# Kernel tuning notes

Hardware: AMD Instinct MI355X
Metric: run time of the kernel (lower is better)

## Reference

```python
import jax, jax.numpy as jnp
import numpy as np

NODE_SIZE = 30000
REL_SIZE = 1000
TRIPLE_SIZE = 200000
DIM = 128
DEPTH = 2
BATCH = 2048
GAMMA = 3.0
LAMB, TAU = 30.0, 10.0


def glorot(k, shape):
    lim = np.sqrt(6.0 / (shape[-2] + shape[-1]))
    return jax.random.uniform(k, shape, minval=-lim, maxval=lim, dtype=jnp.float32)


def setup_inputs() -> dict:
    key = jax.random.key(0)
    ks = jax.random.split(key, 12)
    train_paris = jax.random.randint(ks[0], (BATCH, 2), 0, NODE_SIZE, dtype=jnp.int32)
    ent_adj = jax.random.randint(ks[1], (2, TRIPLE_SIZE), 0, NODE_SIZE, dtype=jnp.int32)
    rel_adj = jnp.stack([
        jax.random.randint(ks[2], (TRIPLE_SIZE,), 0, NODE_SIZE, dtype=jnp.int32),
        jax.random.randint(ks[3], (TRIPLE_SIZE,), 0, REL_SIZE, dtype=jnp.int32),
    ])
    adj_list = jax.random.randint(ks[4], (2, TRIPLE_SIZE), 0, NODE_SIZE, dtype=jnp.int32)
    r_index = jnp.stack([
        jnp.arange(TRIPLE_SIZE, dtype=jnp.int32),
        jax.random.randint(ks[5], (TRIPLE_SIZE,), 0, REL_SIZE, dtype=jnp.int32),
    ])
    r_val = jax.random.uniform(ks[6], (TRIPLE_SIZE,), dtype=jnp.float32)
    mask = jnp.ones((TRIPLE_SIZE,), jnp.float32)
    ent_emb = glorot(ks[7], (NODE_SIZE, DIM))
    rel_emb = glorot(ks[8], (REL_SIZE, DIM))
    attn_e = glorot(ks[9], (DEPTH, DIM, 1))
    attn_r = glorot(ks[10], (DEPTH, DIM, 1))
    return dict(train_paris=train_paris, ent_adj=ent_adj, rel_adj=rel_adj,
                adj_list=adj_list, r_index=r_index, r_val=r_val, mask=mask,
                ent_emb=ent_emb, rel_emb=rel_emb, attn_e=attn_e, attn_r=attn_r,
                node_size=NODE_SIZE, rel_size=REL_SIZE, triple_size=TRIPLE_SIZE)


def sparse_mean(adj, emb, num_rows):
    # torch.sparse.softmax over all-ones values == 1/deg per row, then sparse mm == mean aggregation
    rows, cols = adj[0], adj[1]
    s = jax.ops.segment_sum(emb[cols], rows, num_segments=num_rows)
    cnt = jax.ops.segment_sum(jnp.ones(rows.shape, emb.dtype), rows, num_segments=num_rows)
    return s / jnp.maximum(cnt, 1.0)[:, None]


def segment_softmax(logits, seg, num_segments):
    m = jax.lax.stop_gradient(jax.ops.segment_max(logits, seg, num_segments=num_segments))
    e = jnp.exp(logits - m[seg])
    z = jax.ops.segment_sum(e, seg, num_segments=num_segments)
    return e / z[seg]


def nr_gat(features, rel_emb, adj_list, r_index, r_val, attn_kernels, node_size, triple_size):
    # RREA-style NR_GraphAttention: relation-aware reflection + segment softmax attention
    feats = jnp.tanh(features)
    outs = [feats]
    # tri_rel[t] = sum_r r_val * rel_emb[r] for entries (t, r); here one relation per triple
    tri_rel = jax.ops.segment_sum(r_val[:, None] * rel_emb[r_index[1]], r_index[0],
                                  num_segments=triple_size)
    tri_rel = tri_rel / jnp.maximum(jnp.linalg.norm(tri_rel, axis=1, keepdims=True), 1e-12)
    rows, cols = adj_list[0], adj_list[1]
    for l in range(DEPTH):
        neighs = feats[cols]  # [T, D]
        # Householder reflection across normalized relation vector
        neighs = neighs - 2.0 * jnp.sum(neighs * tri_rel, axis=1, keepdims=True) * tri_rel
        att = jnp.squeeze(tri_rel @ attn_kernels[l], axis=-1)  # [T]
        w = segment_softmax(att, rows, node_size)
        feats = jnp.tanh(jax.ops.segment_sum(w[:, None] * neighs, rows, num_segments=node_size))
        outs.append(feats)
    return jnp.concatenate(outs, axis=1)  # [N, (depth+1)*D]


def align_loss(pairs, emb, node_size):
    l, r = pairs[:, 0], pairs[:, 1]
    l_emb, r_emb = emb[l], emb[r]
    pos = jnp.sum(jnp.square(l_emb - r_emb), axis=-1, keepdims=True)  # [B,1]
    emb_sq = jnp.sum(emb * emb, axis=1)  # [N]

    def sqdist(A):
        return jnp.sum(A * A, axis=1, keepdims=True) + emb_sq[None, :] - 2.0 * (A @ emb.T)

    b = pairs.shape[0]
    rows = jnp.arange(b)
    factor = jnp.ones((b, node_size), emb.dtype).at[rows, l].add(-1.0).at[rows, r].add(-1.0)

    def branch(neg):
        loss = (pos - neg + GAMMA) * factor
        mu = jax.lax.stop_gradient(jnp.mean(loss, axis=-1, keepdims=True))
        sd = jax.lax.stop_gradient(jnp.std(loss, axis=-1, keepdims=True))
        return jax.nn.logsumexp(LAMB * (loss - mu) / sd + TAU, axis=-1)

    return jnp.mean(branch(sqdist(l_emb)) + branch(sqdist(r_emb)))


def reference(train_paris, ent_adj, rel_adj, adj_list, r_index, r_val, mask,
              ent_emb, rel_emb, attn_e, attn_r, node_size, rel_size, triple_size):
    # gcn_forward: mean aggregation of entity / relation embeddings (sparse softmax of ones + spmm)
    ent_feature = sparse_mean(ent_adj, ent_emb, node_size)
    rel_feature = sparse_mean(rel_adj, rel_emb, node_size)
    e_out = nr_gat(ent_feature, rel_emb, adj_list, r_index, r_val, attn_e, node_size, triple_size)
    r_out = nr_gat(rel_feature, rel_emb, adj_list, r_index, r_val, attn_r, node_size, triple_size)
    out_feature = jnp.concatenate([e_out, r_out], axis=-1)  # [N, 2*(depth+1)*D]; dropout rate 0 -> identity
    return align_loss(train_paris, out_feature, node_size)
```

## Files before the change

kernel.cpp:

```cpp
#include <hip/hip_runtime.h>
#include <hip/hip_bf16.h>
#include <math.h>

#define N_NODE 30000
#define N_TRI  200000
#define DIM    128
#define OUTD   768
#define BATCH  2048
#define NROWA  4096
#define EPAD   30080
#define PADN   80
#define NTILE_E 235
#define NTILE_A 32
#define NCHB   16
#define NBLK_SCAN 118
#define TILE_ELEMS (128*OUTD)
#define KBLK_ELEMS (128*32)
#define GAMMA_C 3.0f
#define LAMB_C  30.0f
#define TAU_C   10.0f

typedef __attribute__((ext_vector_type(8)))  __bf16 bf16x8;
typedef __attribute__((ext_vector_type(4)))  __bf16 bf16x4;
typedef __attribute__((ext_vector_type(2)))  __bf16 bf16x2;
typedef __attribute__((ext_vector_type(8)))  _Float16 half8;
typedef __attribute__((ext_vector_type(4)))  float f32x4;

__device__ __forceinline__ float waveSum(float v){
#pragma unroll
  for (int m=1;m<64;m<<=1) v += __shfl_xor(v, m, 64);
  return v;
}
__device__ __forceinline__ float halfSum(float v){
#pragma unroll
  for (int m=1;m<32;m<<=1) v += __shfl_xor(v, m, 64);
  return v;
}

__device__ __forceinline__ void atomicMinF(float* a, float v){
  if (v >= 0.f) atomicMin((int*)a, __float_as_int(v));
  else          atomicMax((unsigned int*)a, __float_as_uint(v));
}

__device__ __forceinline__ void gl2lds16(const void* g, void* l){
  __builtin_amdgcn_global_load_lds(
      (const __attribute__((address_space(1))) char*)g,
      (__attribute__((address_space(3))) char*)l, 16, 0, 0);
}

__device__ __forceinline__ int swz_off(int r, int q){
  return r*32 + ((q ^ ((r>>1)&3))<<3);
}

__global__ void k_fill(float* __restrict__ p, long n, float v){
  long i = (long)blockIdx.x*blockDim.x + threadIdx.x;
  long st = (long)gridDim.x*blockDim.x;
  for (; i<n; i+=st) p[i]=v;
}

__global__ __launch_bounds__(256) void k_hist(const int* __restrict__ rows, int* __restrict__ cnt){
  int t = blockIdx.x*256 + threadIdx.x;
  if (t < N_TRI) atomicAdd(&cnt[rows[t]], 1);
}

__global__ __launch_bounds__(256) void k_scanA(
    const int* __restrict__ c0, const int* __restrict__ c1, const int* __restrict__ c2,
    int* __restrict__ r0, int* __restrict__ r1, int* __restrict__ r2,
    int* __restrict__ btot, int n){
  const int* cnt = blockIdx.y==0 ? c0 : (blockIdx.y==1 ? c1 : c2);
  int* rp        = blockIdx.y==0 ? r0 : (blockIdx.y==1 ? r1 : r2);
  __shared__ int buf[256];
  int i = blockIdx.x*256 + threadIdx.x;
  int v = (i<n) ? cnt[i] : 0;
  buf[threadIdx.x] = v;
  __syncthreads();
  for (int off=1; off<256; off<<=1){
    int t = (threadIdx.x>=off) ? buf[threadIdx.x-off] : 0;
    __syncthreads();
    buf[threadIdx.x] += t;
    __syncthreads();
  }
  if (i<n) rp[i] = buf[threadIdx.x] - v;
  if (threadIdx.x==255) btot[blockIdx.y*NBLK_SCAN + blockIdx.x] = buf[255];
}

__global__ __launch_bounds__(128) void k_scanB(int* __restrict__ btot,
    int* __restrict__ r0, int* __restrict__ r1, int* __restrict__ r2, int n){
  __shared__ int buf[128];
  int c = blockIdx.x;
  int v = (threadIdx.x < NBLK_SCAN) ? btot[c*NBLK_SCAN + threadIdx.x] : 0;
  buf[threadIdx.x] = v;
  __syncthreads();
  for (int off=1; off<128; off<<=1){
    int t = (threadIdx.x>=off) ? buf[threadIdx.x-off] : 0;
    __syncthreads();
    buf[threadIdx.x] += t;
    __syncthreads();
  }
  if (threadIdx.x < NBLK_SCAN) btot[c*NBLK_SCAN + threadIdx.x] = buf[threadIdx.x] - v;
  if (threadIdx.x == 127){
    int* rp = c==0 ? r0 : (c==1 ? r1 : r2);
    rp[n] = buf[127];
  }
}

__global__ __launch_bounds__(256) void k_scanC(
    int* __restrict__ r0, int* __restrict__ r1, int* __restrict__ r2,
    const int* __restrict__ btot, int n){
  int* rp = blockIdx.y==0 ? r0 : (blockIdx.y==1 ? r1 : r2);
  int i = blockIdx.x*256 + threadIdx.x;
  if (i<n) rp[i] += btot[blockIdx.y*NBLK_SCAN + blockIdx.x];
}

__global__ __launch_bounds__(256) void k_place(const int* __restrict__ rows, const int* __restrict__ vals,
                        const int* __restrict__ rowptr, int* __restrict__ cur, int* __restrict__ idx, int mode){
  int t = blockIdx.x*256 + threadIdx.x;
  if (t < N_TRI){
    int r = rows[t];
    int p = atomicAdd(&cur[r], 1);
    idx[rowptr[r] + p] = mode ? vals[t] : t;
  }
}

__global__ __launch_bounds__(256) void k_feat0(
    const int* __restrict__ rpE, const int* __restrict__ idxE,
    const int* __restrict__ rpR, const int* __restrict__ idxR,
    const float* __restrict__ ent_emb, const float* __restrict__ rel_emb,
    __bf16* __restrict__ outb){
  int wave = threadIdx.x>>6, lane = threadIdx.x&63;
  int i = blockIdx.x*4 + wave;
  if (i >= N_NODE) return;
  int bE = rpE[i], eE = rpE[i+1];
  int bR = rpR[i], eR = rpR[i+1];
  float2 aE = {0.f,0.f}, aR = {0.f,0.f};
  for (int k=bE; k<eE; ++k){
    int c = idxE[k];
    float2 v = *(const float2*)(ent_emb + (size_t)c*DIM + lane*2);
    aE.x += v.x; aE.y += v.y;
  }
  for (int k=bR; k<eR; ++k){
    int c = idxR[k];
    float2 v = *(const float2*)(rel_emb + (size_t)c*DIM + lane*2);
    aR.x += v.x; aR.y += v.y;
  }
  float ie = 1.f/fmaxf((float)(eE-bE), 1.f);
  float ir = 1.f/fmaxf((float)(eR-bR), 1.f);
  bf16x2 oE, oR;
  oE[0] = (__bf16)tanhf(aE.x*ie); oE[1] = (__bf16)tanhf(aE.y*ie);
  oR[0] = (__bf16)tanhf(aR.x*ir); oR[1] = (__bf16)tanhf(aR.y*ir);
  *(bf16x2*)(outb + (size_t)i*OUTD +   0 + lane*2) = oE;
  *(bf16x2*)(outb + (size_t)i*OUTD + 128 + lane*2) = oR;
}

__global__ __launch_bounds__(256) void k_trinorm(
    const int* __restrict__ ridx1, const float* __restrict__ rval,
    const float* __restrict__ rel_emb,
    __bf16* __restrict__ tri, const float* __restrict__ attnE,
    const float* __restrict__ attnR, float* __restrict__ att4){
  __shared__ float ak[4][DIM];
  int tid = threadIdx.x;
  for (int idx=tid; idx<4*DIM; idx+=256){
    int k = idx>>7, d = idx&127;
    ak[k][d] = (k<2) ? attnE[k*DIM + d] : attnR[(k-2)*DIM + d];
  }
  __syncthreads();
  int half = tid>>5, l31 = tid&31;
  int t = blockIdx.x*8 + half;
  if (t >= N_TRI) return;
  int rr = ridx1[t];
  float rv = rval[t];
  float4 v = *(const float4*)(rel_emb + (size_t)rr*DIM + l31*4);
  v.x *= rv; v.y *= rv; v.z *= rv; v.w *= rv;
  float ss = halfSum(v.x*v.x + v.y*v.y + v.z*v.z + v.w*v.w);
  float inv = 1.f/fmaxf(sqrtf(ss), 1e-12f);
  v.x *= inv; v.y *= inv; v.z *= inv; v.w *= inv;
  bf16x4 b; b[0]=(__bf16)v.x; b[1]=(__bf16)v.y; b[2]=(__bf16)v.z; b[3]=(__bf16)v.w;
  *(bf16x4*)(tri + (size_t)t*DIM + l31*4) = b;
#pragma unroll
  for (int k=0;k<4;k++){
    const float* a = &ak[k][l31*4];
    float p = halfSum(v.x*a[0] + v.y*a[1] + v.z*a[2] + v.w*a[3]);
    if (l31==0) att4[(size_t)k*N_TRI + t] = p;
  }
}

__global__ __launch_bounds__(256) void k_gat(
    const int* __restrict__ rowptr, const int* __restrict__ idx, const int* __restrict__ cols,
    const __bf16* __restrict__ tri,
    const float* __restrict__ attE, const float* __restrict__ attR,
    __bf16* __restrict__ outb, int inOff, int outOff){
  int wave = threadIdx.x>>6, lane = threadIdx.x&63;
  int i = blockIdx.x*4 + wave;
  if (i >= N_NODE) return;
  int l31 = lane&31;
  const float* att = (lane < 32) ? attE : attR;
  int beg = rowptr[i], end = rowptr[i+1];
  float a0=0.f, a1=0.f, a2=0.f, a3=0.f;
  if (end > beg){
    float z = 0.f;
    int t0 = idx[beg];
    int c0 = cols[t0];
    bf16x4 u4 = *(const bf16x4*)(tri + (size_t)t0*DIM + l31*4);
    bf16x4 f4 = *(const bf16x4*)(outb + (size_t)c0*OUTD + inOff + lane*4);
    float atv = att[t0];
    for (int k=beg; k<end; ++k){
      bf16x4 u4c = u4, f4c = f4;
      float atc = atv;
      if (k+1 < end){
        int t1 = idx[k+1];
        int c1 = cols[t1];
        u4 = *(const bf16x4*)(tri + (size_t)t1*DIM + l31*4);
        f4 = *(const bf16x4*)(outb + (size_t)c1*OUTD + inOff + lane*4);
        atv = att[t1];
      }
      float u0=(float)u4c[0], u1=(float)u4c[1], u2=(float)u4c[2], u3=(float)u4c[3];
      float f0=(float)f4c[0], f1=(float)f4c[1], f2=(float)f4c[2], f3=(float)f4c[3];
      float d = f0*u0 + f1*u1 + f2*u2 + f3*u3;
#pragma unroll
      for (int mm=1; mm<32; mm<<=1) d += __shfl_xor(d, mm, 64);
      float w = __expf(atc);
      z += w;
      float d2 = 2.f*d;
      a0 = fmaf(w, fmaf(-d2, u0, f0), a0);
      a1 = fmaf(w, fmaf(-d2, u1, f1), a1);
      a2 = fmaf(w, fmaf(-d2, u2, f2), a2);
      a3 = fmaf(w, fmaf(-d2, u3, f3), a3);
    }
    float iz = 1.f/z;
    a0 *= iz; a1 *= iz; a2 *= iz; a3 *= iz;
  }
  bf16x4 o;
  o[0] = (__bf16)tanhf(a0); o[1] = (__bf16)tanhf(a1);
  o[2] = (__bf16)tanhf(a2); o[3] = (__bf16)tanhf(a3);
  *(bf16x4*)(outb + (size_t)i*OUTD + outOff + lane*4) = o;
}

__global__ __launch_bounds__(256) void k_packE(const __bf16* __restrict__ outb, __bf16* __restrict__ Ep, float* __restrict__ esq){
  const int perm[6] = {0,2,4,1,3,5};
  int wave = threadIdx.x>>6, lane = threadIdx.x&63;
  int j = blockIdx.x*4 + wave;
  if (j >= EPAD) return;
  int jt = j>>7, r = j&127;
  __bf16* tb = Ep + (size_t)jt*TILE_ELEMS;
  float ss = 0.f;
  for (int c=lane; c<96; c+=64){
    int kb = c>>2, q = c&3;
    bf16x8 o;
    if (j < N_NODE){
      int ib = perm[c>>4], wb = c&15;
      o = *(const bf16x8*)(outb + (size_t)j*OUTD + ib*128 + wb*8);
#pragma unroll
      for (int e=0;e<8;e++){ float v = (float)o[e]; ss += v*v; }
    } else {
#pragma unroll
      for (int e=0;e<8;e++) o[e] = (__bf16)0.f;
    }
    *(bf16x8*)(tb + kb*KBLK_ELEMS + swz_off(r, q)) = o;
  }
  ss = waveSum(ss);
  if (lane==0) esq[j] = (j < N_NODE) ? ss : 0.f;
}

__global__ __launch_bounds__(256) void k_packA(const int* __restrict__ pairs, const __bf16* __restrict__ Ep,
    const __bf16* __restrict__ outb, const float* __restrict__ esq,
    __bf16* __restrict__ Ap, float* __restrict__ asq, float* __restrict__ pos){
  int wave = threadIdx.x>>6, lane = threadIdx.x&63;
  int p = blockIdx.x*4 + wave;
  if (p >= BATCH) return;
  int l = pairs[2*p], r = pairs[2*p+1];
  float ss = 0.f;
#pragma unroll
  for (int c=0;c<6;c++){
    int d = c*128 + lane*2;
    bf16x2 a = *(const bf16x2*)(outb + (size_t)l*OUTD + d);
    bf16x2 b = *(const bf16x2*)(outb + (size_t)r*OUTD + d);
    float dx = (float)a[0]-(float)b[0], dy = (float)a[1]-(float)b[1];
    ss += dx*dx + dy*dy;
  }
  ss = waveSum(ss);
  if (lane==0){ pos[p] = ss; asq[p] = esq[l]; asq[p+BATCH] = esq[r]; }
  int lt = l>>7, lr = l&127;
  int rt2 = r>>7, rr = r&127;
  int p0t = p>>7, p0r = p&127;
  int p1t = (p+BATCH)>>7, p1r = (p+BATCH)&127;
  for (int c=lane; c<96; c+=64){
    int kb = c>>2, q = c&3;
    bf16x8 vl = *(const bf16x8*)(Ep + (size_t)lt*TILE_ELEMS + kb*KBLK_ELEMS + swz_off(lr, q));
    *(bf16x8*)(Ap + (size_t)p0t*TILE_ELEMS + kb*KBLK_ELEMS + swz_off(p0r, q)) = vl;
    bf16x8 vr = *(const bf16x8*)(Ep + (size_t)rt2*TILE_ELEMS + kb*KBLK_ELEMS + swz_off(rr, q));
    *(bf16x8*)(Ap + (size_t)p1t*TILE_ELEMS + kb*KBLK_ELEMS + swz_off(p1r, q)) = vr;
  }
}

__global__ __launch_bounds__(256) void k_gemm(
    const __bf16* __restrict__ Ap, const __bf16* __restrict__ Ep,
    const float* __restrict__ asq, const float* __restrict__ esq,
    const int* __restrict__ pairs,
    float* __restrict__ rs1, float* __restrict__ rs2, float* __restrict__ rmin,
    _Float16* __restrict__ neg16, int biOff)
{
  __shared__ char smem[49152];
  __bf16* sA = (__bf16*)smem;
  __bf16* sB = (__bf16*)(smem + 16384);
  int tid = threadIdx.x;

  int wave = tid>>6, lane = tid&63, quad = lane>>4, l16 = lane&15;
  int biL = blockIdx.x, bj = blockIdx.y;
  int bi = biOff + biL;
  int wi = wave>>1, wj = wave&1;

  const __bf16* Asrc = Ap + (size_t)bi*TILE_ELEMS;
  const __bf16* Bsrc = Ep + (size_t)bj*TILE_ELEMS;

  int a_off[4], b_off[4];
#pragma unroll
  for (int rt=0; rt<4; ++rt){ int row = wi*64 + rt*16 + l16; a_off[rt] = swz_off(row, quad); }
#pragma unroll
  for (int ct=0; ct<4; ++ct){ int row = wj*64 + ct*16 + l16; b_off[ct] = swz_off(row, quad); }

  const __bf16* gsrc = (wave<2 ? Asrc : Bsrc);
  __bf16* ldsb = (wave<2 ? sA : sB);
  int half = (wave&1)*KBLK_ELEMS;

  const f32x4 zf = {0.f,0.f,0.f,0.f};
  f32x4 acc[4][4];
#pragma unroll
  for (int rt=0; rt<4; ++rt)
#pragma unroll
    for (int ct=0; ct<4; ++ct) acc[rt][ct] = zf;

  for (int kb2=0; kb2<12; ++kb2){
    __syncthreads();
    const __bf16* g = gsrc + kb2*(2*KBLK_ELEMS) + half + lane*8;
#pragma unroll
    for (int s=0; s<8; ++s)
      gl2lds16(g + s*512, ldsb + half + s*512);
    __syncthreads();
#pragma unroll
    for (int ks=0; ks<2; ++ks){
      int o = ks*KBLK_ELEMS;
      bf16x8 af[4], bf[4];
#pragma unroll
      for (int rt=0; rt<4; ++rt) af[rt] = *(const bf16x8*)(sA + o + a_off[rt]);
#pragma unroll
      for (int ct=0; ct<4; ++ct) bf[ct] = *(const bf16x8*)(sB + o + b_off[ct]);
#pragma unroll
      for (int rt=0; rt<4; ++rt)
#pragma unroll
        for (int ct=0; ct<4; ++ct)
          acc[rt][ct] = __builtin_amdgcn_mfma_f32_16x16x32_bf16(af[rt], bf[ct], acc[rt][ct], 0,0,0);
    }
  }

  int jbase = bj*128 + wj*64;
  float esqv[4]; bool val[4]; int jcol[4];
#pragma unroll
  for (int ct=0; ct<4; ++ct){
    jcol[ct] = jbase + ct*16 + l16;
    val[ct] = jcol[ct] < N_NODE;
    esqv[ct] = esq[jcol[ct]];
  }

  __syncthreads();
  float* red = (float*)smem;
  int col = wj*16 + l16;

  size_t tBase = ((size_t)bj*NCHB + biL)*16384;
#pragma unroll
  for (int rt=0; rt<4; ++rt){
    _Float16 h16[16];
#pragma unroll
    for (int reg=0; reg<4; ++reg){
      int il = wi*64 + rt*16 + quad*4 + reg;
      int i  = bi*128 + il;
      int p  = i & (BATCH-1);
      int li = pairs[2*p], ri = pairs[2*p+1];
      float av = asq[i];
      float s=0.f, q=0.f, mn=1e30f;
#pragma unroll
      for (int ct=0; ct<4; ++ct){
        float neg = (av + esqv[ct]) - 2.f*acc[rt][ct][reg];
        s += neg;
        q = fmaf(neg, neg, q);
        bool bad = (jcol[ct]==li) | (jcol[ct]==ri) | (!val[ct]);
        mn = fminf(mn, bad ? 1e30f : neg);
        h16[reg*4+ct] = (_Float16)neg;
      }
      red[        il*32 + col] = s;
      red[4096 +  il*32 + col] = q;
      red[8192 +  il*32 + col] = mn;
    }
    _Float16* dst = neg16 + tBase + ((size_t)(wave*4 + rt))*1024 + lane*16;
    *(half8*)(dst)     = *(half8*)&h16[0];
    *(half8*)(dst + 8) = *(half8*)&h16[8];
  }
  __syncthreads();
  if (tid < 128){
    int il = tid;
    float s = 0.f, q = 0.f, mn = 1e30f;
#pragma unroll
    for (int c4=0; c4<8; ++c4){
      f32x4 sv = *(f32x4*)&red[il*32 + c4*4];
      s += sv[0]+sv[1]+sv[2]+sv[3];
    }
#pragma unroll
    for (int c4=0; c4<8; ++c4){
      f32x4 qv = *(f32x4*)&red[4096 + il*32 + c4*4];
      q += qv[0]+qv[1]+qv[2]+qv[3];
    }
#pragma unroll
    for (int c4=0; c4<8; ++c4){
      f32x4 mv = *(f32x4*)&red[8192 + il*32 + c4*4];
      mn = fminf(mn, fminf(fminf(mv[0],mv[1]), fminf(mv[2],mv[3])));
    }
    int i = bi*128 + il;
    atomicAdd(rs1+i, s);
    atomicAdd(rs2+i, q);
    atomicMinF(rmin+i, mn);
  }
}

__global__ __launch_bounds__(256) void k_p2s(
    const _Float16* __restrict__ neg16, const float* __restrict__ CC, const float* __restrict__ AL,
    const int* __restrict__ pairs, float* __restrict__ rexp, int biOff)
{
  __shared__ float red[256];
  int tid = threadIdx.x;
  int wave = tid>>6, lane = tid&63, quad = lane>>4, l16 = lane&15;
  int biL = blockIdx.x, bj = blockIdx.y;
  int bi = biOff + biL;
  int wi = wave>>1, wj = wave&1;
  int jbase = bj*128 + wj*64;
  bool val[4]; int jcol[4];
#pragma unroll
  for (int ct=0; ct<4; ++ct){
    jcol[ct] = jbase + ct*16 + l16;
    val[ct] = jcol[ct] < N_NODE;
  }
  size_t tBase = ((size_t)bj*NCHB + biL)*16384;
#pragma unroll
  for (int rt=0; rt<4; ++rt){
    const _Float16* src = neg16 + tBase + ((size_t)(wave*4 + rt))*1024 + lane*16;
    half8 v0 = *(const half8*)(src);
    half8 v1 = *(const half8*)(src + 8);
    _Float16 h16[16];
    *(half8*)&h16[0] = v0; *(half8*)&h16[8] = v1;
#pragma unroll
    for (int reg=0; reg<4; ++reg){
      int il = wi*64 + rt*16 + quad*4 + reg;
      int i  = bi*128 + il;
      int p  = i & (BATCH-1);
      int li = pairs[2*p], ri = pairs[2*p+1];
      float C = CC[i], A = AL[i];
      float s = 0.f;
#pragma unroll
      for (int ct=0; ct<4; ++ct){
        float neg = (float)h16[reg*4+ct];
        bool bad = (jcol[ct]==li) | (jcol[ct]==ri) | (!val[ct]);
        s += bad ? 0.f : __expf(fmaf(-A, neg, C));
      }
#pragma unroll
      for (int m=1;m<16;m<<=1) s += __shfl_xor(s,m,64);
      if (l16 == 0) red[il*2+wj] = s;
    }
  }
  __syncthreads();
  if (tid < 128){
    int i = bi*128 + tid;
    atomicAdd(rexp+i, red[tid*2] + red[tid*2+1]);
  }
}

__global__ __launch_bounds__(256) void k_corr(
    const int* __restrict__ pairs, const __bf16* __restrict__ Ap, const __bf16* __restrict__ Ep,
    const float* __restrict__ asq, const float* __restrict__ esq,
    float* __restrict__ negl, float* __restrict__ negr, int iOff)
{
  int wave = threadIdx.x>>6, lane = threadIdx.x&63;
  int i = iOff + blockIdx.x*4 + wave;
  int p = i & (BATCH-1);
  int li = pairs[2*p], ri = pairs[2*p+1];
  const __bf16* Ar = Ap + (size_t)(i>>7)*TILE_ELEMS;  int ra = i&127;
  const __bf16* E1 = Ep + (size_t)(li>>7)*TILE_ELEMS; int r1 = li&127;
  const __bf16* E2 = Ep + (size_t)(ri>>7)*TILE_ELEMS; int r2 = ri&127;
  float d1=0.f, d2=0.f;
  for (int c=lane; c<96; c+=64){
    int kb = c>>2, q = c&3;
    bf16x8 a  = *(const bf16x8*)(Ar + kb*KBLK_ELEMS + swz_off(ra, q));
    bf16x8 e1 = *(const bf16x8*)(E1 + kb*KBLK_ELEMS + swz_off(r1, q));
    bf16x8 e2 = *(const bf16x8*)(E2 + kb*KBLK_ELEMS + swz_off(r2, q));
#pragma unroll
    for (int e=0;e<8;e++){
      d1 = fmaf((float)a[e], (float)e1[e], d1);
      d2 = fmaf((float)a[e], (float)e2[e], d2);
    }
  }
  d1 = waveSum(d1); d2 = waveSum(d2);
  if (lane==0){
    float av = asq[i];
    negl[i] = av + esq[li] - 2.f*d1;
    negr[i] = av + esq[ri] - 2.f*d2;
  }
}

__global__ __launch_bounds__(256) void k_stats(
    const float* __restrict__ rs1, const float* __restrict__ rs2, const float* __restrict__ rmin,
    const float* __restrict__ negl, const float* __restrict__ negr,
    const float* __restrict__ asq, const float* __restrict__ pos, const int* __restrict__ pairs,
    float* __restrict__ MM, float* __restrict__ CC, float* __restrict__ AL, float* __restrict__ rexp, int iOff)
{
  int i = iOff + blockIdx.x*256 + threadIdx.x;
  int p = i & (BATCH-1);
  int li = pairs[2*p], ri = pairs[2*p+1];
  float K = pos[p] + GAMMA_C;
  float av = asq[i];
  float S1 = rs1[i] - (float)PADN*av;
  float S2 = rs2[i] - (float)PADN*av*av;
  float nl = negl[i], nr = negr[i];
  float Sx, Sxx, mx;
  const float invN = 1.f/(float)N_NODE;
  if (li != ri){
    Sx  = -(S1 - nl - nr) - 2.f*K;
    Sxx = (S2 - nl*nl - nr*nr) + 2.f*K*K;
    mx  = fmaxf(K - rmin[i], 0.f);
    float mu = K + Sx*invN;
    float m2 = Sx*invN;
    float var = Sxx*invN - m2*m2;
    float sd = sqrtf(fmaxf(var, 1e-30f));
    float M = LAMB_C*(mx-mu)/sd + TAU_C;
    MM[i] = M; CC[i] = LAMB_C*(K-mu)/sd + TAU_C - M; AL[i] = LAMB_C/sd;
    rexp[i] = 2.f*__expf(LAMB_C*(0.f-mu)/sd + TAU_C - M);
  } else {
    float lossm = nl - K;
    float x = lossm - K;
    Sx  = -(S1 - nl) + x;
    Sxx = (S2 - nl*nl) + x*x;
    mx  = fmaxf(K - rmin[i], lossm);
    float mu = K + Sx*invN;
    float m2 = Sx*invN;
    float var = Sxx*invN - m2*m2;
    float sd = sqrtf(fmaxf(var, 1e-30f));
    float M = LAMB_C*(mx-mu)/sd + TAU_C;
    MM[i] = M; CC[i] = LAMB_C*(K-mu)/sd + TAU_C - M; AL[i] = LAMB_C/sd;
    rexp[i] = __expf(LAMB_C*(lossm-mu)/sd + TAU_C - M);
  }
}

__global__ __launch_bounds__(256) void k_final(const float* __restrict__ mm, const float* __restrict__ rexp, float* __restrict__ out){
  __shared__ float red[256];
  float s = 0.f;
  for (int i=threadIdx.x; i<NROWA; i+=256) s += mm[i] + logf(rexp[i]);
  red[threadIdx.x] = s; __syncthreads();
  for (int st=128; st>0; st>>=1){ if (threadIdx.x<st) red[threadIdx.x]+=red[threadIdx.x+st]; __syncthreads(); }
  if (threadIdx.x==0) out[0] = red[0]*(1.f/BATCH);
}

extern "C" void kernel_launch(void* const* d_in, const int* in_sizes, int n_in,
                              void* d_out, int out_size, void* d_ws, size_t ws_size,
                              hipStream_t stream) {
  const int*   pairs   = (const int*)d_in[0];
  const int*   ent_adj = (const int*)d_in[1];
  const int*   rel_adj = (const int*)d_in[2];
  const int*   adj     = (const int*)d_in[3];
  const int*   r_index = (const int*)d_in[4];
  const float* r_val   = (const float*)d_in[5];
  const float* ent_emb = (const float*)d_in[7];
  const float* rel_emb = (const float*)d_in[8];
  const float* attn_e  = (const float*)d_in[9];
  const float* attn_r  = (const float*)d_in[10];

  char* base = (char*)d_ws;
  size_t off = 0;
  auto take = [&](size_t bytes)->char*{
    char* p = base + off;
    off = (off + bytes + 511) & ~(size_t)511;
    return p;
  };
  __bf16* EP    = (__bf16*)take((size_t)NTILE_E*TILE_ELEMS*2);
  __bf16* AP    = (__bf16*)take((size_t)NTILE_A*TILE_ELEMS*2);
  float*  ESQ   = (float*)take((size_t)EPAD*4);
  float*  ASQ   = (float*)take((size_t)NROWA*4);
  float*  POS   = (float*)take((size_t)BATCH*4);
  float*  RS1   = (float*)take((size_t)NROWA*4);
  float*  RS2   = (float*)take((size_t)NROWA*4);
  float*  RMIN  = (float*)take((size_t)NROWA*4);
  float*  NEGL  = (float*)take((size_t)NROWA*4);
  float*  NEGR  = (float*)take((size_t)NROWA*4);
  float*  MM    = (float*)take((size_t)NROWA*4);
  float*  CCv   = (float*)take((size_t)NROWA*4);
  float*  ALv   = (float*)take((size_t)NROWA*4);
  float*  REXP  = (float*)take((size_t)NROWA*4);

  size_t offG = off;
  __bf16* OUTB = (__bf16*)take((size_t)N_NODE*OUTD*2);
  __bf16* TRI  = (__bf16*)take((size_t)N_TRI*DIM*2);
  float*  ATT4 = (float*)take((size_t)4*N_TRI*4);
  int* RP_E  = (int*)take((size_t)(N_NODE+1)*4);
  int* RP_R  = (int*)take((size_t)(N_NODE+1)*4);
  int* RP_A  = (int*)take((size_t)(N_NODE+1)*4);
  int* IDX_E = (int*)take((size_t)N_TRI*4);
  int* IDX_R = (int*)take((size_t)N_TRI*4);
  int* IDX_A = (int*)take((size_t)N_TRI*4);
  int* CNT6  = (int*)take((size_t)6*N_NODE*4);
  int* BTOT  = (int*)take((size_t)3*NBLK_SCAN*4);
  int* CNT_E = CNT6,            *CNT_R = CNT6 + N_NODE,   *CNT_A = CNT6 + 2*N_NODE;
  int* CUR_E = CNT6 + 3*N_NODE, *CUR_R = CNT6 + 4*N_NODE, *CUR_A = CNT6 + 5*N_NODE;

  _Float16* NEG16 = (_Float16*)(base + offG);

  const int* cols = adj + N_TRI;

  k_fill<<<192,256,0,stream>>>((float*)CNT6, (long)6*N_NODE, 0.f);

  k_hist<<<782,256,0,stream>>>(ent_adj, CNT_E);
  k_hist<<<782,256,0,stream>>>(rel_adj, CNT_R);
  k_hist<<<782,256,0,stream>>>(adj,     CNT_A);
  dim3 gsA(NBLK_SCAN, 3, 1);
  k_scanA<<<gsA,256,0,stream>>>(CNT_E, CNT_R, CNT_A, RP_E, RP_R, RP_A, BTOT, N_NODE);
  k_scanB<<<3,128,0,stream>>>(BTOT, RP_E, RP_R, RP_A, N_NODE);
  k_scanC<<<gsA,256,0,stream>>>(RP_E, RP_R, RP_A, BTOT, N_NODE);
  k_place<<<782,256,0,stream>>>(ent_adj, ent_adj+N_TRI, RP_E, CUR_E, IDX_E, 1);
  k_place<<<782,256,0,stream>>>(rel_adj, rel_adj+N_TRI, RP_R, CUR_R, IDX_R, 1);
  k_place<<<782,256,0,stream>>>(adj,     (const int*)0, RP_A, CUR_A, IDX_A, 0);

  k_feat0<<<7500,256,0,stream>>>(RP_E, IDX_E, RP_R, IDX_R, ent_emb, rel_emb, OUTB);
  k_trinorm<<<25000,256,0,stream>>>(r_index+N_TRI, r_val, rel_emb, TRI, attn_e, attn_r, ATT4);
  k_gat<<<7500,256,0,stream>>>(RP_A, IDX_A, cols, TRI,
                               ATT4 + 0*N_TRI, ATT4 + 2*N_TRI, OUTB, 0, 256);
  k_gat<<<7500,256,0,stream>>>(RP_A, IDX_A, cols, TRI,
                               ATT4 + 1*N_TRI, ATT4 + 3*N_TRI, OUTB, 256, 512);

  k_packE<<<7520,256,0,stream>>>(OUTB, EP, ESQ);
  k_packA<<<512,256,0,stream>>>(pairs, EP, OUTB, ESQ, AP, ASQ, POS);
  k_fill<<<16,256,0,stream>>>(RS1, (long)NROWA, 0.f);
  k_fill<<<16,256,0,stream>>>(RS2, (long)NROWA, 0.f);
  k_fill<<<16,256,0,stream>>>(RMIN,(long)NROWA, 1e30f);

  for (int ch=0; ch<NTILE_A/NCHB; ++ch){
    int biOff = ch*NCHB;
    int iOff  = biOff*128;
    dim3 gg(NCHB, NTILE_E, 1);
    k_gemm<<<gg,256,0,stream>>>(AP, EP, ASQ, ESQ, pairs, RS1, RS2, RMIN, NEG16, biOff);
    k_corr<<<NCHB*128/4,256,0,stream>>>(pairs, AP, EP, ASQ, ESQ, NEGL, NEGR, iOff);
    k_stats<<<NCHB*128/256,256,0,stream>>>(RS1, RS2, RMIN, NEGL, NEGR, ASQ, POS, pairs,
                                           MM, CCv, ALv, REXP, iOff);
    k_p2s<<<gg,256,0,stream>>>(NEG16, CCv, ALv, pairs, REXP, biOff);
  }
  k_final<<<1,256,0,stream>>>(MM, REXP, (float*)d_out);
}
```

Before: 694.8 us.

## Use 256x256 GEMM tiles with double-buffered LDS and interleaved prefetch

```diff
diff --git a/kernel.cpp b/kernel.cpp
--- a/kernel.cpp
+++ b/kernel.cpp
@@ -8,11 +8,12 @@
 #define OUTD   768
 #define BATCH  2048
 #define NROWA  4096
-#define EPAD   30080
-#define PADN   80
-#define NTILE_E 235
+#define EPAD   30208
+#define PADN   208
+#define NTILE_E 236
 #define NTILE_A 32
-#define NCHB   16
+#define NTILE_EJ 118
+#define NTILE_AI 8
 #define NBLK_SCAN 118
 #define TILE_ELEMS (128*OUTD)
 #define KBLK_ELEMS (128*32)
@@ -292,182 +293,240 @@
   }
 }
 
-__global__ __launch_bounds__(256) void k_gemm(
+__global__ __launch_bounds__(512,2) void k_gemm(
     const __bf16* __restrict__ Ap, const __bf16* __restrict__ Ep,
     const float* __restrict__ asq, const float* __restrict__ esq,
     const int* __restrict__ pairs,
     float* __restrict__ rs1, float* __restrict__ rs2, float* __restrict__ rmin,
     _Float16* __restrict__ neg16, int biOff)
 {
-  __shared__ char smem[49152];
-  __bf16* sA = (__bf16*)smem;
-  __bf16* sB = (__bf16*)(smem + 16384);
-  int tid = threadIdx.x;
-
-  int wave = tid>>6, lane = tid&63, quad = lane>>4, l16 = lane&15;
-  int biL = blockIdx.x, bj = blockIdx.y;
-  int bi = biOff + biL;
-  int wi = wave>>1, wj = wave&1;
-
-  const __bf16* Asrc = Ap + (size_t)bi*TILE_ELEMS;
-  const __bf16* Bsrc = Ep + (size_t)bj*TILE_ELEMS;
-
-  int a_off[4], b_off[4];
-#pragma unroll
-  for (int rt=0; rt<4; ++rt){ int row = wi*64 + rt*16 + l16; a_off[rt] = swz_off(row, quad); }
-#pragma unroll
-  for (int ct=0; ct<4; ++ct){ int row = wj*64 + ct*16 + l16; b_off[ct] = swz_off(row, quad); }
-
-  const __bf16* gsrc = (wave<2 ? Asrc : Bsrc);
-  __bf16* ldsb = (wave<2 ? sA : sB);
-  int half = (wave&1)*KBLK_ELEMS;
+  __shared__ __align__(16) char smem[143360];
+  const int tid = threadIdx.x;
+  const int w = tid>>6, lane = tid&63, quad = lane>>4, l16 = lane&15;
+  const int wr = w>>2, wc = w&3;
+
+  int wg = blockIdx.x*NTILE_EJ + blockIdx.y;
+  const int biL = wg & 7;
+  const int bj  = wg >> 3;
+  const int bi  = biOff + biL;
+
+  const __bf16* Abase = Ap + (size_t)(bi*2)*TILE_ELEMS;
+  const __bf16* Bbase = Ep + (size_t)(bj*2)*TILE_ELEMS;
+
+  const int s0b = swz_off(l16, quad)*2;
+  const int aBase = wr*16384 + s0b;
+  const int bBase = 32768 + (wc>>1)*16384 + (wc&1)*4096 + s0b;
 
   const f32x4 zf = {0.f,0.f,0.f,0.f};
-  f32x4 acc[4][4];
-#pragma unroll
-  for (int rt=0; rt<4; ++rt)
-#pragma unroll
-    for (int ct=0; ct<4; ++ct) acc[rt][ct] = zf;
-
-  for (int kb2=0; kb2<12; ++kb2){
-    __syncthreads();
-    const __bf16* g = gsrc + kb2*(2*KBLK_ELEMS) + half + lane*8;
-#pragma unroll
-    for (int s=0; s<8; ++s)
-      gl2lds16(g + s*512, ldsb + half + s*512);
-    __syncthreads();
-#pragma unroll
-    for (int ks=0; ks<2; ++ks){
-      int o = ks*KBLK_ELEMS;
-      bf16x8 af[4], bf[4];
-#pragma unroll
-      for (int rt=0; rt<4; ++rt) af[rt] = *(const bf16x8*)(sA + o + a_off[rt]);
-#pragma unroll
-      for (int ct=0; ct<4; ++ct) bf[ct] = *(const bf16x8*)(sB + o + b_off[ct]);
-#pragma unroll
-      for (int rt=0; rt<4; ++rt)
-#pragma unroll
-        for (int ct=0; ct<4; ++ct)
-          acc[rt][ct] = __builtin_amdgcn_mfma_f32_16x16x32_bf16(af[rt], bf[ct], acc[rt][ct], 0,0,0);
-    }
-  }
-
-  int jbase = bj*128 + wj*64;
-  float esqv[4]; bool val[4]; int jcol[4];
-#pragma unroll
-  for (int ct=0; ct<4; ++ct){
-    jcol[ct] = jbase + ct*16 + l16;
-    val[ct] = jcol[ct] < N_NODE;
-    esqv[ct] = esq[jcol[ct]];
-  }
-
-  __syncthreads();
-  float* red = (float*)smem;
-  int col = wj*16 + l16;
-
-  size_t tBase = ((size_t)bj*NCHB + biL)*16384;
-#pragma unroll
-  for (int rt=0; rt<4; ++rt){
+  f32x4 acc[8][4];
+#pragma unroll
+  for (int m=0;m<8;m++)
+#pragma unroll
+    for (int n=0;n<4;n++) acc[m][n] = zf;
+
+  auto stageA = [&](int t, int rt){
+    const __bf16* src = Abase + (size_t)rt*TILE_ELEMS + (size_t)(t*2)*KBLK_ELEMS + tid*8;
+    char* dst = smem + (t&1)*65536 + rt*16384 + tid*16;
+    gl2lds16(src, dst);
+    gl2lds16(src + KBLK_ELEMS, dst + 8192);
+  };
+  auto stageB = [&](int t, int rt){
+    const __bf16* src = Bbase + (size_t)rt*TILE_ELEMS + (size_t)(t*2)*KBLK_ELEMS + tid*8;
+    char* dst = smem + (t&1)*65536 + 32768 + rt*16384 + tid*16;
+    gl2lds16(src, dst);
+    gl2lds16(src + KBLK_ELEMS, dst + 8192);
+  };
+
+  stageB(0,0); stageB(0,1); stageA(0,0); stageA(0,1); stageB(1,0); stageB(1,1);
+  asm volatile("s_waitcnt vmcnt(4)" ::: "memory");
+  __builtin_amdgcn_s_barrier();
+
+  bf16x8 aF[4][2], bF[2][2][2];
+
+#pragma unroll 1
+  for (int t=0; t<12; ++t){
+    const char* bufc = smem + (t&1)*65536;
+
+#pragma unroll
+    for (int m4=0;m4<4;m4++)
+#pragma unroll
+      for (int ks=0;ks<2;ks++)
+        aF[m4][ks] = *(const bf16x8*)(bufc + aBase + ks*8192 + m4*1024);
+#pragma unroll
+    for (int n2=0;n2<2;n2++)
+#pragma unroll
+      for (int ks=0;ks<2;ks++)
+        bF[0][n2][ks] = *(const bf16x8*)(bufc + bBase + ks*8192 + n2*1024);
+    if (t+1<12) stageA(t+1, 0);
+    __builtin_amdgcn_s_barrier();
+    __builtin_amdgcn_s_setprio(1);
+#pragma unroll
+    for (int m4=0;m4<4;m4++)
+#pragma unroll
+      for (int n2=0;n2<2;n2++)
+#pragma unroll
+        for (int ks=0;ks<2;ks++)
+          acc[m4][n2] = __builtin_amdgcn_mfma_f32_16x16x32_bf16(aF[m4][ks], bF[0][n2][ks], acc[m4][n2],0,0,0);
+    __builtin_amdgcn_s_setprio(0);
+    __builtin_amdgcn_s_barrier();
+
+#pragma unroll
+    for (int n2=0;n2<2;n2++)
+#pragma unroll
+      for (int ks=0;ks<2;ks++)
+        bF[1][n2][ks] = *(const bf16x8*)(bufc + bBase + ks*8192 + (2+n2)*1024);
+    if (t+1<12) stageA(t+1, 1);
+    __builtin_amdgcn_s_barrier();
+    __builtin_amdgcn_s_setprio(1);
+#pragma unroll
+    for (int m4=0;m4<4;m4++)
+#pragma unroll
+      for (int n2=0;n2<2;n2++)
+#pragma unroll
+        for (int ks=0;ks<2;ks++)
+          acc[m4][2+n2] = __builtin_amdgcn_mfma_f32_16x16x32_bf16(aF[m4][ks], bF[1][n2][ks], acc[m4][2+n2],0,0,0);
+    __builtin_amdgcn_s_setprio(0);
+    __builtin_amdgcn_s_barrier();
+
+#pragma unroll
+    for (int m4=0;m4<4;m4++)
+#pragma unroll
+      for (int ks=0;ks<2;ks++)
+        aF[m4][ks] = *(const bf16x8*)(bufc + aBase + ks*8192 + (4+m4)*1024);
+    if (t+2<12) stageB(t+2, 0);
+    __builtin_amdgcn_s_barrier();
+    __builtin_amdgcn_s_setprio(1);
+#pragma unroll
+    for (int m4=0;m4<4;m4++)
+#pragma unroll
+      for (int n2=0;n2<2;n2++)
+#pragma unroll
+        for (int ks=0;ks<2;ks++)
+          acc[4+m4][n2] = __builtin_amdgcn_mfma_f32_16x16x32_bf16(aF[m4][ks], bF[0][n2][ks], acc[4+m4][n2],0,0,0);
+    __builtin_amdgcn_s_setprio(0);
+    __builtin_amdgcn_s_barrier();
+
+    if (t+2<12) stageB(t+2, 1);
+    __builtin_amdgcn_s_setprio(1);
+#pragma unroll
+    for (int m4=0;m4<4;m4++)
+#pragma unroll
+      for (int n2=0;n2<2;n2++)
+#pragma unroll
+        for (int ks=0;ks<2;ks++)
+          acc[4+m4][2+n2] = __builtin_amdgcn_mfma_f32_16x16x32_bf16(aF[m4][ks], bF[1][n2][ks], acc[4+m4][2+n2],0,0,0);
+    __builtin_amdgcn_s_setprio(0);
+    if (t < 10) asm volatile("s_waitcnt vmcnt(4)" ::: "memory");
+    else        asm volatile("s_waitcnt vmcnt(0)" ::: "memory");
+    __builtin_amdgcn_s_barrier();
+  }
+
+  float* redS = (float*)(smem + 131072);
+  int jcol[4]; bool val[4]; float esqv[4];
+#pragma unroll
+  for (int n=0;n<4;n++){
+    jcol[n] = bj*256 + wc*64 + n*16 + l16;
+    val[n] = jcol[n] < N_NODE;
+    esqv[n] = esq[jcol[n]];
+  }
+  const int rowB = bi*256;
+  size_t tBase = ((size_t)bj*8 + biL)*65536;
+#pragma unroll
+  for (int m=0;m<8;m++){
     _Float16 h16[16];
 #pragma unroll
-    for (int reg=0; reg<4; ++reg){
-      int il = wi*64 + rt*16 + quad*4 + reg;
-      int i  = bi*128 + il;
-      int p  = i & (BATCH-1);
+    for (int reg=0;reg<4;reg++){
+      int il = wr*128 + m*16 + quad*4 + reg;
+      int i = rowB + il;
+      int p = i & (BATCH-1);
       int li = pairs[2*p], ri = pairs[2*p+1];
       float av = asq[i];
       float s=0.f, q=0.f, mn=1e30f;
 #pragma unroll
-      for (int ct=0; ct<4; ++ct){
-        float neg = (av + esqv[ct]) - 2.f*acc[rt][ct][reg];
+      for (int n=0;n<4;n++){
+        float neg = (av + esqv[n]) - 2.f*acc[m][n][reg];
         s += neg;
         q = fmaf(neg, neg, q);
-        bool bad = (jcol[ct]==li) | (jcol[ct]==ri) | (!val[ct]);
+        bool bad = (jcol[n]==li) | (jcol[n]==ri) | (!val[n]);
         mn = fminf(mn, bad ? 1e30f : neg);
-        h16[reg*4+ct] = (_Float16)neg;
+        h16[reg*4+n] = (_Float16)neg;
       }
-      red[        il*32 + col] = s;
-      red[4096 +  il*32 + col] = q;
-      red[8192 +  il*32 + col] = mn;
+#pragma unroll
+      for (int msk=1; msk<16; msk<<=1){
+        s += __shfl_xor(s, msk, 64);
+        q += __shfl_xor(q, msk, 64);
+        mn = fminf(mn, __shfl_xor(mn, msk, 64));
+      }
+      if (l16==0){
+        redS[       il*4 + wc] = s;
+        redS[1024 + il*4 + wc] = q;
+        redS[2048 + il*4 + wc] = mn;
+      }
     }
-    _Float16* dst = neg16 + tBase + ((size_t)(wave*4 + rt))*1024 + lane*16;
+    _Float16* dst = neg16 + tBase + ((size_t)(w*8 + m))*1024 + lane*16;
     *(half8*)(dst)     = *(half8*)&h16[0];
     *(half8*)(dst + 8) = *(half8*)&h16[8];
   }
   __syncthreads();
-  if (tid < 128){
-    int il = tid;
-    float s = 0.f, q = 0.f, mn = 1e30f;
-#pragma unroll
-    for (int c4=0; c4<8; ++c4){
-      f32x4 sv = *(f32x4*)&red[il*32 + c4*4];
-      s += sv[0]+sv[1]+sv[2]+sv[3];
-    }
-#pragma unroll
-    for (int c4=0; c4<8; ++c4){
-      f32x4 qv = *(f32x4*)&red[4096 + il*32 + c4*4];
-      q += qv[0]+qv[1]+qv[2]+qv[3];
-    }
-#pragma unroll
-    for (int c4=0; c4<8; ++c4){
-      f32x4 mv = *(f32x4*)&red[8192 + il*32 + c4*4];
-      mn = fminf(mn, fminf(fminf(mv[0],mv[1]), fminf(mv[2],mv[3])));
-    }
-    int i = bi*128 + il;
-    atomicAdd(rs1+i, s);
-    atomicAdd(rs2+i, q);
-    atomicMinF(rmin+i, mn);
-  }
-}
-
-__global__ __launch_bounds__(256) void k_p2s(
+  if (tid < 256){
+    int i = rowB + tid;
+    f32x4 sv = *(f32x4*)&redS[tid*4];
+    f32x4 qv = *(f32x4*)&redS[1024 + tid*4];
+    f32x4 mv = *(f32x4*)&redS[2048 + tid*4];
+    atomicAdd(rs1+i, sv[0]+sv[1]+sv[2]+sv[3]);
+    atomicAdd(rs2+i, qv[0]+qv[1]+qv[2]+qv[3]);
+    atomicMinF(rmin+i, fminf(fminf(mv[0],mv[1]), fminf(mv[2],mv[3])));
+  }
+}
+
+__global__ __launch_bounds__(512) void k_p2s(
     const _Float16* __restrict__ neg16, const float* __restrict__ CC, const float* __restrict__ AL,
     const int* __restrict__ pairs, float* __restrict__ rexp, int biOff)
 {
-  __shared__ float red[256];
-  int tid = threadIdx.x;
-  int wave = tid>>6, lane = tid&63, quad = lane>>4, l16 = lane&15;
-  int biL = blockIdx.x, bj = blockIdx.y;
-  int bi = biOff + biL;
-  int wi = wave>>1, wj = wave&1;
-  int jbase = bj*128 + wj*64;
-  bool val[4]; int jcol[4];
-#pragma unroll
-  for (int ct=0; ct<4; ++ct){
-    jcol[ct] = jbase + ct*16 + l16;
-    val[ct] = jcol[ct] < N_NODE;
-  }
-  size_t tBase = ((size_t)bj*NCHB + biL)*16384;
-#pragma unroll
-  for (int rt=0; rt<4; ++rt){
-    const _Float16* src = neg16 + tBase + ((size_t)(wave*4 + rt))*1024 + lane*16;
+  __shared__ float red[1024];
+  const int tid = threadIdx.x;
+  const int w = tid>>6, lane = tid&63, quad = lane>>4, l16 = lane&15;
+  const int wr = w>>2, wc = w&3;
+  const int biL = blockIdx.x, bj = blockIdx.y;
+  const int bi = biOff + biL;
+  const int rowB = bi*256;
+  int jcol[4]; bool val[4];
+#pragma unroll
+  for (int n=0;n<4;n++){
+    jcol[n] = bj*256 + wc*64 + n*16 + l16;
+    val[n] = jcol[n] < N_NODE;
+  }
+  size_t tBase = ((size_t)bj*8 + biL)*65536;
+#pragma unroll
+  for (int m=0;m<8;m++){
+    const _Float16* src = neg16 + tBase + ((size_t)(w*8 + m))*1024 + lane*16;
     half8 v0 = *(const half8*)(src);
     half8 v1 = *(const half8*)(src + 8);
     _Float16 h16[16];
     *(half8*)&h16[0] = v0; *(half8*)&h16[8] = v1;
 #pragma unroll
-    for (int reg=0; reg<4; ++reg){
-      int il = wi*64 + rt*16 + quad*4 + reg;
-      int i  = bi*128 + il;
-      int p  = i & (BATCH-1);
+    for (int reg=0;reg<4;reg++){
+      int il = wr*128 + m*16 + quad*4 + reg;
+      int i = rowB + il;
+      int p = i & (BATCH-1);
       int li = pairs[2*p], ri = pairs[2*p+1];
       float C = CC[i], A = AL[i];
       float s = 0.f;
 #pragma unroll
-      for (int ct=0; ct<4; ++ct){
-        float neg = (float)h16[reg*4+ct];
-        bool bad = (jcol[ct]==li) | (jcol[ct]==ri) | (!val[ct]);
+      for (int n=0;n<4;n++){
+        float neg = (float)h16[reg*4+n];
+        bool bad = (jcol[n]==li) | (jcol[n]==ri) | (!val[n]);
         s += bad ? 0.f : __expf(fmaf(-A, neg, C));
       }
 #pragma unroll
-      for (int m=1;m<16;m<<=1) s += __shfl_xor(s,m,64);
-      if (l16 == 0) red[il*2+wj] = s;
+      for (int msk=1; msk<16; msk<<=1) s += __shfl_xor(s, msk, 64);
+      if (l16==0) red[il*4 + wc] = s;
     }
   }
   __syncthreads();
-  if (tid < 128){
-    int i = bi*128 + tid;
-    atomicAdd(rexp+i, red[tid*2] + red[tid*2+1]);
+  if (tid < 256){
+    f32x4 sv = *(f32x4*)&red[tid*4];
+    atomicAdd(rexp + rowB + tid, sv[0]+sv[1]+sv[2]+sv[3]);
   }
 }
 
@@ -630,21 +689,21 @@
   k_gat<<<7500,256,0,stream>>>(RP_A, IDX_A, cols, TRI,
                                ATT4 + 1*N_TRI, ATT4 + 3*N_TRI, OUTB, 256, 512);
 
-  k_packE<<<7520,256,0,stream>>>(OUTB, EP, ESQ);
+  k_packE<<<7552,256,0,stream>>>(OUTB, EP, ESQ);
   k_packA<<<512,256,0,stream>>>(pairs, EP, OUTB, ESQ, AP, ASQ, POS);
   k_fill<<<16,256,0,stream>>>(RS1, (long)NROWA, 0.f);
   k_fill<<<16,256,0,stream>>>(RS2, (long)NROWA, 0.f);
   k_fill<<<16,256,0,stream>>>(RMIN,(long)NROWA, 1e30f);
 
-  for (int ch=0; ch<NTILE_A/NCHB; ++ch){
-    int biOff = ch*NCHB;
-    int iOff  = biOff*128;
-    dim3 gg(NCHB, NTILE_E, 1);
-    k_gemm<<<gg,256,0,stream>>>(AP, EP, ASQ, ESQ, pairs, RS1, RS2, RMIN, NEG16, biOff);
-    k_corr<<<NCHB*128/4,256,0,stream>>>(pairs, AP, EP, ASQ, ESQ, NEGL, NEGR, iOff);
-    k_stats<<<NCHB*128/256,256,0,stream>>>(RS1, RS2, RMIN, NEGL, NEGR, ASQ, POS, pairs,
-                                           MM, CCv, ALv, REXP, iOff);
-    k_p2s<<<gg,256,0,stream>>>(NEG16, CCv, ALv, pairs, REXP, biOff);
+  for (int ch=0; ch<2; ++ch){
+    int biOff = ch*NTILE_AI;
+    int iOff  = ch*2048;
+    dim3 gg(NTILE_AI, NTILE_EJ, 1);
+    k_gemm<<<gg,512,0,stream>>>(AP, EP, ASQ, ESQ, pairs, RS1, RS2, RMIN, NEG16, biOff);
+    k_corr<<<512,256,0,stream>>>(pairs, AP, EP, ASQ, ESQ, NEGL, NEGR, iOff);
+    k_stats<<<8,256,0,stream>>>(RS1, RS2, RMIN, NEGL, NEGR, ASQ, POS, pairs,
+                                MM, CCv, ALv, REXP, iOff);
+    k_p2s<<<gg,512,0,stream>>>(NEG16, CCv, ALv, pairs, REXP, biOff);
   }
   k_final<<<1,256,0,stream>>>(MM, REXP, (float*)d_out);
 }
```

Result: slower. 722.1 us (+3.9%).
